# Optimization experiments

Measured on AMD Instinct MI355X. Metric: run time of the kernel, lower is better.

## Reference

```python
import jax, jax.numpy as jnp
import numpy as np

MIN_NORM = 1e-5
EPS = 1e-7
N_NODES = 100000
N_EDGES = 20000
NNZ = 640000
F_DIM = 128  # in_channels == out_channels
NUM_LAYERS = 2
MAX_NORM = 1e6


def _cosh(x):
    return jnp.cosh(jnp.clip(x, -15.0, 15.0))


def _sinh(x):
    return jnp.sinh(jnp.clip(x, -15.0, 15.0))


def _arcosh(x):
    # caller already clamps x >= 1 + eps
    return jnp.log(x + jnp.sqrt(jnp.clip(x * x - 1.0, EPS)))


def proj(x, c):
    K = 1.0 / c
    y = x[:, 1:]
    y_sq = jnp.sum(y * y, axis=1, keepdims=True)
    x0 = jnp.sqrt(jnp.clip(K + y_sq, EPS))
    return jnp.concatenate([x0, y], axis=1)


def proj_tan0(u):
    # zero out the time-like (first) coordinate
    return jnp.concatenate([jnp.zeros_like(u[:, :1]), u[:, 1:]], axis=1)


def expmap0(u, c):
    K = 1.0 / c
    sqrtK = jnp.sqrt(K)
    x = u[:, 1:]
    x_norm = jnp.clip(jnp.linalg.norm(x, axis=1, keepdims=True), MIN_NORM)
    theta = x_norm / sqrtK
    res0 = sqrtK * _cosh(theta)
    res_rest = sqrtK * _sinh(theta) * x / x_norm
    return proj(jnp.concatenate([res0, res_rest], axis=1), c)


def logmap0(x, c):
    K = 1.0 / c
    sqrtK = jnp.sqrt(K)
    y = x[:, 1:]
    y_norm = jnp.clip(jnp.linalg.norm(y, axis=1, keepdims=True), MIN_NORM)
    theta = jnp.clip(x[:, 0:1] / sqrtK, 1.0 + EPS)
    rest = sqrtK * _arcosh(theta) * y / y_norm
    return jnp.concatenate([jnp.zeros_like(x[:, :1]), rest], axis=1)


def minkowski_norm(u):
    dot = jnp.sum(u * u, axis=-1, keepdims=True) - 2.0 * (u[:, 0:1] * u[:, 0:1])
    return jnp.sqrt(jnp.clip(dot, EPS))


def proj_tan(u, x):
    ux = jnp.sum(x[:, 1:] * u[:, 1:], axis=1, keepdims=True)
    v0 = ux / jnp.clip(x[:, 0:1], EPS)
    return jnp.concatenate([v0, u[:, 1:]], axis=1)


def expmap(u, x, c):
    K = 1.0 / c
    sqrtK = jnp.sqrt(K)
    normu = jnp.clip(minkowski_norm(u), None, MAX_NORM)
    theta = jnp.clip(normu / sqrtK, MIN_NORM)
    result = _cosh(theta) * x + _sinh(theta) * u / theta
    return proj(result, c)


def ptransp0(x, u, c):
    K = 1.0 / c
    sqrtK = jnp.sqrt(K)
    x0 = x[:, 0:1]
    y = x[:, 1:]
    y_norm = jnp.clip(jnp.linalg.norm(y, axis=1, keepdims=True), MIN_NORM)
    y_hat = y / y_norm
    v = jnp.concatenate([-y_norm, (sqrtK - x0) * y_hat], axis=1)
    alpha = jnp.sum(y_hat * u[:, 1:], axis=1, keepdims=True) / sqrtK
    res = u - alpha * v
    return proj_tan(res, x)


def mobius_add(x, y, c):
    u = logmap0(y, c)
    v = ptransp0(x, u, c)
    return expmap(v, x, c)


def hyp_block(x, node_idx, edge_idx, bias, c_in, c_out):
    # tangent features at origin
    x = proj_tan0(logmap0(x, c_in))
    # degree normalizations (hyperedge_weight = ones, EW_weight = None)
    ones_nnz = jnp.ones((node_idx.shape[0],), dtype=x.dtype)
    D = jax.ops.segment_sum(ones_nnz, node_idx, num_segments=N_NODES)
    D = jnp.where(D > 0, 1.0 / D, 0.0)
    B = jax.ops.segment_sum(ones_nnz, edge_idx, num_segments=N_EDGES)
    B = jnp.where(B > 0, 1.0 / B, 0.0)
    # propagate nodes -> hyperedges (norm = B at destination edge)
    m1 = B[edge_idx][:, None] * x[node_idx]            # [nnz, F]
    e_feat = jax.ops.segment_sum(m1, edge_idx, num_segments=N_EDGES)
    # propagate hyperedges -> nodes (norm = D at destination node)
    m2 = D[node_idx][:, None] * e_feat[edge_idx]       # [nnz, F]
    out = jax.ops.segment_sum(m2, node_idx, num_segments=N_NODES)
    # hyperbolic bias add + activation
    bias_t = proj_tan0(bias[None, :])
    hyp_bias = proj(expmap0(bias_t, c_in), c_in)
    res = proj(out, c_in)
    res = proj(mobius_add(res, hyp_bias, c_in), c_in)
    out = jax.nn.leaky_relu(logmap0(res, c_in), 0.01)
    out = proj_tan0(out)
    return proj(expmap0(out, c_out), c_out)


def reference(x, hyperedge_index, curvatures, biases):
    node_idx = hyperedge_index[0]
    edge_idx = hyperedge_index[1]
    # encoder: prepend zero time coordinate, lift to hyperboloid
    h = jnp.concatenate([jnp.zeros_like(x[:, :1]), x], axis=1)
    c0 = jax.nn.softplus(curvatures[0])
    h = proj(expmap0(proj_tan0(h), c0), c0)
    for i in range(NUM_LAYERS):
        c_in = jax.nn.softplus(curvatures[i])
        c_out = jax.nn.softplus(curvatures[i + 1])
        h = hyp_block(h, node_idx, edge_idx, biases[i], c_in, c_out)
    # decoder
    c_last = jax.nn.softplus(curvatures[-1])
    return proj_tan0(logmap0(h, c_last))


def setup_inputs() -> dict:
    key = jax.random.key(0)
    k1, k2, k3, k4 = jax.random.split(key, 4)
    x = jax.random.normal(k1, (N_NODES, F_DIM - 1), dtype=jnp.float32)
    node_idx = jax.random.randint(k2, (NNZ,), 0, N_NODES)
    edge_idx = jax.random.randint(k3, (NNZ,), 0, N_EDGES)
    edge_idx = edge_idx.at[-1].set(N_EDGES - 1)  # ensure max edge id = E-1
    hyperedge_index = jnp.stack([node_idx, edge_idx], axis=0).astype(jnp.int64)
    curvatures = jnp.full((NUM_LAYERS + 1,), 0.1, dtype=jnp.float32)
    biases = 0.02 * jax.random.normal(k4, (NUM_LAYERS, F_DIM), dtype=jnp.float32)
    return {"x": x, "hyperedge_index": hyperedge_index, "curvatures": curvatures, "biases": biases}
```

## Files before the change

kernel.cpp:

```cpp
#include <hip/hip_runtime.h>
#include <hip/hip_fp16.h>
#include <math.h>

#define N_NODESc 100000
#define N_EDGESc 20000
#define NNZc     640000
#define FD       128
#define WE       96
#define WN       48
#define NBKT     256
#define EPB      2048
#define NCHUNKS  313
#define ESHIFT   7
#define NSHIFT   9
#define STAGEBLK 6250
#define MIN_NORMf 1e-5f
#define EPSf      1e-7f
#define MAX_NORMf 1e6f

__device__ __forceinline__ float wred(float v){
  #pragma unroll
  for(int m=32;m;m>>=1) v += __shfl_xor(v, m, 64);
  return v;
}
__device__ __forceinline__ void wred2_16(float& a, float& b){
  #pragma unroll
  for(int m=8;m;m>>=1){
    float ta = __shfl_xor(a, m, 64);
    float tb = __shfl_xor(b, m, 64);
    a += ta; b += tb;
  }
}

__device__ __forceinline__ void h8_acc(const float4 h, float4& a0, float4& a1){
  const __half2* hp = (const __half2*)&h;
  float2 f0 = __half22float2(hp[0]);
  float2 f1 = __half22float2(hp[1]);
  float2 f2 = __half22float2(hp[2]);
  float2 f3 = __half22float2(hp[3]);
  a0.x += f0.x; a0.y += f0.y; a0.z += f1.x; a0.w += f1.y;
  a1.x += f2.x; a1.y += f2.y; a1.z += f3.x; a1.w += f3.y;
}
__device__ __forceinline__ float4 pack_h8(const float4 a, const float4 b){
  float4 out;
  __half2* hp = (__half2*)&out;
  hp[0] = __float22half2_rn(make_float2(a.x,a.y));
  hp[1] = __float22half2_rn(make_float2(a.z,a.w));
  hp[2] = __float22half2_rn(make_float2(b.x,b.y));
  hp[3] = __float22half2_rn(make_float2(b.z,b.w));
  return out;
}

__device__ __forceinline__ void get_pair(const int* hei, int k, int f64, int& n, int& e){
  if(f64){ n = hei[2*k]; e = hei[2*NNZc + 2*k]; }
  else   { n = hei[k];   e = hei[NNZc + k]; }
}

__global__ void k_prep(const int* hei, const float* curv, const float* biases,
                       int* flag, float* scal, float* ubias, int* gHist){
  int tid = threadIdx.x;
  gHist[tid] = 0;
  gHist[tid + NBKT] = 0;
  if(tid < 64){
    int lane = tid;
    int hi = hei[2*lane+1];
    unsigned long long b = __ballot(hi != 0);
    if(lane==0) flag[0] = (b==0ull) ? 1 : 0;
    if(lane==0){
      scal[0] = log1pf(expf(curv[0]));
      scal[1] = log1pf(expf(curv[1]));
      scal[2] = log1pf(expf(curv[2]));
    }
    int d0 = 2*lane, d1 = d0+1;
    for(int L=0; L<2; ++L){
      float u0 = (d0==0) ? 0.f : biases[L*FD + d0];
      float u1 = biases[L*FD + d1];
      ubias[L*FD + d0] = u0;
      ubias[L*FD + d1] = u1;
      float uu = wred(u0*u0 + u1*u1);
      if(lane==0) scal[3+L] = uu;
    }
  }
}

__global__ void k_stage_hist(const float* x, float4* xh,
                             const int* hei, const int* flag, int* gHist){
  int bid = blockIdx.x;
  if(bid < STAGEBLK){
    int t = bid*256 + threadIdx.x;
    int node = t >> 4, l16 = t & 15;
    int d8 = 8*l16;
    const float* r = x + (size_t)node*(FD-1);
    float4 p0, p1;
    if(l16==0){
      float4 q0 = *(const float4*)(r);
      p1 = *(const float4*)(r + 3);
      p0 = make_float4(0.f, q0.x, q0.y, q0.z);
    } else {
      p0 = *(const float4*)(r + d8 - 1);
      p1 = *(const float4*)(r + d8 + 3);
    }
    xh[(size_t)node*16 + l16] = pack_h8(p0, p1);
  } else {
    __shared__ int h[NBKT];
    int tid = threadIdx.x;
    int hb = bid - STAGEBLK;
    int side = hb & 1;
    int chunk = hb >> 1;
    h[tid] = 0; __syncthreads();
    int f64 = flag[0];
    int base = chunk*EPB;
    #pragma unroll
    for(int j=0;j<8;++j){
      int k = base + j*256 + tid;
      if(k < NNZc){
        int n,e; get_pair(hei,k,f64,n,e);
        int b = side ? (n>>NSHIFT) : (e>>ESHIFT);
        atomicAdd(&h[b],1);
      }
    }
    __syncthreads();
    int c = h[tid];
    if(c>0) atomicAdd(&gHist[side*NBKT+tid], c);
  }
}

__global__ void k_scan(const int* gHist, int* gCur){
  __shared__ int sd[NBKT];
  int tid = threadIdx.x;
  for(int s=0;s<2;++s){
    int v = gHist[s*NBKT+tid];
    sd[tid]=v; __syncthreads();
    for(int off=1; off<NBKT; off<<=1){
      int t = (tid>=off)? sd[tid-off] : 0;
      __syncthreads();
      sd[tid] += t;
      __syncthreads();
    }
    gCur[s*NBKT+tid] = sd[tid]-v;
    __syncthreads();
  }
}

__global__ void k_part(const int* hei, const int* flag, int* gCur,
                       unsigned long long* partE, unsigned long long* partN,
                       int* curE, int* curN){
  int gtid = blockIdx.x*blockDim.x + threadIdx.x;
  if(gtid < N_EDGESc) curE[gtid] = 0;
  else if(gtid < N_EDGESc + N_NODESc) curN[gtid - N_EDGESc] = 0;

  __shared__ int h[NBKT];
  __shared__ int bbase[NBKT];
  int tid = threadIdx.x;
  int side = blockIdx.x & 1;
  int chunk = blockIdx.x >> 1;
  h[tid]=0; __syncthreads();
  int f64 = flag[0];
  int base = chunk*EPB;
  int keyv[8], payl[8], rank[8], bkt[8];
  #pragma unroll
  for(int j=0;j<8;++j){
    int k = base + j*256 + tid;
    if(k < NNZc){
      int n,e; get_pair(hei,k,f64,n,e);
      if(side==0){ keyv[j]=e; payl[j]=n; bkt[j]=e>>ESHIFT; }
      else       { keyv[j]=n; payl[j]=e; bkt[j]=n>>NSHIFT; }
      rank[j] = atomicAdd(&h[bkt[j]],1);
    } else bkt[j] = -1;
  }
  __syncthreads();
  int c = h[tid];
  if(c>0) bbase[tid] = atomicAdd(&gCur[side*NBKT+tid], c);
  __syncthreads();
  unsigned long long* part = side ? partN : partE;
  #pragma unroll
  for(int j=0;j<8;++j){
    if(bkt[j]>=0){
      int pos = bbase[bkt[j]] + rank[j];
      part[pos] = ((unsigned long long)(unsigned)keyv[j]<<32) | (unsigned)payl[j];
    }
  }
}

__global__ void k_build(const unsigned long long* partE, const unsigned long long* partN,
                        int* curE, int* curN, int* eEll, int* nEll){
  int bid = blockIdx.x;
  int xcd = bid & 7, i = bid >> 3;
  const int q = 1250/8, r = 1250%8;
  int chunk = (xcd<r ? xcd*(q+1) : r*(q+1)+(xcd-r)*q) + i;
  int side = chunk >= 625;
  int c = side ? chunk-625 : chunk;
  const unsigned long long* part = side ? partN : partE;
  int* cur = side ? curN : curE;
  int* ell = side ? nEll : eEll;
  int W = side ? WN : WE;
  int tid = threadIdx.x;
  #pragma unroll
  for(int j=0;j<4;++j){
    int k = c*1024 + j*256 + tid;
    unsigned long long v = part[k];
    int key = (int)(v>>32);
    int pay = (int)(unsigned)v;
    int pos = atomicAdd(&cur[key],1);
    if(pos<W) ell[(size_t)key*W+pos] = pay;
  }
}

__global__ void k_edge_gather(const int* curE, const int* eEll, const float4* rowsH, float4* efeatH){
  int t = blockIdx.x*blockDim.x + threadIdx.x;
  int w    = t >> 6;
  int lane = t & 63;
  int quad = lane >> 4, l16 = lane & 15;
  int edge = w*2 + (quad>>1);
  int qh   = quad & 1;

  int cnt = curE[edge];
  int use = cnt<WE ? cnt : WE;
  const int* ent = eEll + (size_t)edge*WE;

  float4 aA = make_float4(0.f,0.f,0.f,0.f);
  float4 aB = make_float4(0.f,0.f,0.f,0.f);
  int j = qh;
  for(; j+14 < use; j += 16){
    int r0 = ent[j];    int r1 = ent[j+2];
    int r2 = ent[j+4];  int r3 = ent[j+6];
    int r4 = ent[j+8];  int r5 = ent[j+10];
    int r6 = ent[j+12]; int r7 = ent[j+14];
    float4 h0 = rowsH[(size_t)r0*16 + l16];
    float4 h1 = rowsH[(size_t)r1*16 + l16];
    float4 h2 = rowsH[(size_t)r2*16 + l16];
    float4 h3 = rowsH[(size_t)r3*16 + l16];
    float4 h4 = rowsH[(size_t)r4*16 + l16];
    float4 h5 = rowsH[(size_t)r5*16 + l16];
    float4 h6 = rowsH[(size_t)r6*16 + l16];
    float4 h7 = rowsH[(size_t)r7*16 + l16];
    h8_acc(h0,aA,aB); h8_acc(h1,aA,aB); h8_acc(h2,aA,aB); h8_acc(h3,aA,aB);
    h8_acc(h4,aA,aB); h8_acc(h5,aA,aB); h8_acc(h6,aA,aB); h8_acc(h7,aA,aB);
  }
  for(; j < use; j += 2){
    float4 h = rowsH[(size_t)ent[j]*16 + l16];
    h8_acc(h,aA,aB);
  }
  aA.x += __shfl_xor(aA.x, 16, 64); aA.y += __shfl_xor(aA.y, 16, 64);
  aA.z += __shfl_xor(aA.z, 16, 64); aA.w += __shfl_xor(aA.w, 16, 64);
  aB.x += __shfl_xor(aB.x, 16, 64); aB.y += __shfl_xor(aB.y, 16, 64);
  aB.z += __shfl_xor(aB.z, 16, 64); aB.w += __shfl_xor(aB.w, 16, 64);

  if(qh==0){
    float b = cnt>0 ? __fdividef(1.f,(float)cnt) : 0.f;
    aA.x*=b; aA.y*=b; aA.z*=b; aA.w*=b;
    aB.x*=b; aB.y*=b; aB.z*=b; aB.w*=b;
    efeatH[(size_t)edge*16 + l16] = pack_h8(aA, aB);
  }
}

template<int OUTH>
__global__ void k_node_epilogue(const int* curN, const int* nEll, const float4* efeatH,
                                const float* scal, const float* ubias, int layer,
                                float4* outH, float* outF){
  int t = blockIdx.x*blockDim.x + threadIdx.x;
  int w    = t >> 6;
  int lane = t & 63;
  if(w >= N_NODESc/4) return;
  int quad = lane >> 4, l16 = lane & 15;
  int node = w*4 + quad;
  int d8 = 8*l16;

  float cin = scal[layer];
  float K   = __fdividef(1.f, cin);
  float sK  = sqrtf(K);
  float isK = __fdividef(1.f, sK);
  float uu  = scal[3+layer];

  int cnt = curN[node];
  float dv = cnt>0 ? __fdividef(1.f,(float)cnt) : 0.f;
  int use = cnt<WN ? cnt : WN;
  const int* ent = nEll + (size_t)node*WN;

  float4 aA = make_float4(0.f,0.f,0.f,0.f);
  float4 aB = make_float4(0.f,0.f,0.f,0.f);
  int j = 0;
  for(; j+3 < use; j += 4){
    int r0 = ent[j];   int r1 = ent[j+1];
    int r2 = ent[j+2]; int r3 = ent[j+3];
    float4 h0 = efeatH[(size_t)r0*16 + l16];
    float4 h1 = efeatH[(size_t)r1*16 + l16];
    float4 h2 = efeatH[(size_t)r2*16 + l16];
    float4 h3 = efeatH[(size_t)r3*16 + l16];
    h8_acc(h0,aA,aB); h8_acc(h1,aA,aB); h8_acc(h2,aA,aB); h8_acc(h3,aA,aB);
  }
  for(; j < use; ++j){
    float4 h = efeatH[(size_t)ent[j]*16 + l16];
    h8_acc(h,aA,aB);
  }
  aA.x*=dv; aA.y*=dv; aA.z*=dv; aA.w*=dv;
  aB.x*=dv; aB.y*=dv; aB.z*=dv; aB.w*=dv;

  const float4* up = (const float4*)(ubias + layer*FD + d8);
  float4 uA = up[0], uB = up[1];

  float ysq   = aA.x*aA.x + aA.y*aA.y + aA.z*aA.z + aA.w*aA.w
              + aB.x*aB.x + aB.y*aB.y + aB.z*aB.z + aB.w*aB.w;
  float dotAU = aA.x*uA.x + aA.y*uA.y + aA.z*uA.z + aA.w*uA.w
              + aB.x*uB.x + aB.y*uB.y + aB.z*uB.z + aB.w*uB.w;
  wred2_16(ysq, dotAU);

  float res0  = sqrtf(fmaxf(K + ysq, EPSf));
  float ynorm = fmaxf(sqrtf(ysq), MIN_NORMf);
  float iyn   = __fdividef(1.f, ynorm);

  float alpha = dotAU*iyn*isK;
  float ab    = alpha*(sK - res0);
  float abiyn = ab*iyn;
  float4 rA, rB;
  rA.x = fmaf(-abiyn, aA.x, uA.x); rA.y = fmaf(-abiyn, aA.y, uA.y);
  rA.z = fmaf(-abiyn, aA.z, uA.z); rA.w = fmaf(-abiyn, aA.w, uA.w);
  rB.x = fmaf(-abiyn, aB.x, uB.x); rB.y = fmaf(-abiyn, aB.y, uB.y);
  rB.z = fmaf(-abiyn, aB.z, uB.z); rB.w = fmaf(-abiyn, aB.w, uB.w);
  float ux  = fmaf(-ab, ynorm, dotAU);
  float v0s = ux * __fdividef(1.f, fmaxf(res0, EPSf));
  float rsq = fmaf(ab, ab, fmaf(-2.f*abiyn, dotAU, uu));

  float mink  = fmaxf(fmaf(-v0s, v0s, rsq), EPSf);
  float normu = fminf(sqrtf(mink), MAX_NORMf);
  float th    = fmaxf(normu*isK, MIN_NORMf);
  float thc   = fminf(th, 15.f);
  float e  = __expf(thc);
  float ei = __fdividef(1.f, e);
  float ch = 0.5f*(e + ei);
  float sh = 0.5f*(e - ei);
  float sth = sh*__fdividef(1.f, th);
  float4 qA, qB;
  qA.x = fmaf(ch, aA.x, sth*rA.x); qA.y = fmaf(ch, aA.y, sth*rA.y);
  qA.z = fmaf(ch, aA.z, sth*rA.z); qA.w = fmaf(ch, aA.w, sth*rA.w);
  qB.x = fmaf(ch, aB.x, sth*rB.x); qB.y = fmaf(ch, aB.y, sth*rB.y);
  qB.z = fmaf(ch, aB.z, sth*rB.z); qB.w = fmaf(ch, aB.w, sth*rB.w);

  float ysq2 = fmaxf(ch*ch*ysq + 2.f*ch*sth*ux + sth*sth*rsq, 0.f);
  float h0   = sqrtf(fmaxf(K + ysq2, EPSf));
  float yn3  = fmaxf(sqrtf(ysq2), MIN_NORMf);
  float th3  = fmaxf(h0*isK, 1.f+EPSf);
  float acs  = __logf(th3 + sqrtf(fmaxf(fmaf(th3,th3,-1.f), EPSf)));
  float fac  = sK*acs*__fdividef(1.f, yn3);
  float4 tA, tB;
  tA.x = fac*qA.x; tA.y = fac*qA.y; tA.z = fac*qA.z; tA.w = fac*qA.w;
  tB.x = fac*qB.x; tB.y = fac*qB.y; tB.z = fac*qB.z; tB.w = fac*qB.w;
  tA.x = tA.x>=0.f ? tA.x : 0.01f*tA.x;
  tA.y = tA.y>=0.f ? tA.y : 0.01f*tA.y;
  tA.z = tA.z>=0.f ? tA.z : 0.01f*tA.z;
  tA.w = tA.w>=0.f ? tA.w : 0.01f*tA.w;
  tB.x = tB.x>=0.f ? tB.x : 0.01f*tB.x;
  tB.y = tB.y>=0.f ? tB.y : 0.01f*tB.y;
  tB.z = tB.z>=0.f ? tB.z : 0.01f*tB.z;
  tB.w = tB.w>=0.f ? tB.w : 0.01f*tB.w;
  if(l16==0) tA.x = 0.f;

  if(OUTH){
    outH[(size_t)node*16 + l16] = pack_h8(tA, tB);
  } else {
    float4* op = (float4*)(outF + (size_t)node*FD + d8);
    op[0] = tA;
    op[1] = tB;
  }
}

extern "C" void kernel_launch(void* const* d_in, const int* in_sizes, int n_in,
                              void* d_out, int out_size, void* d_ws, size_t ws_size,
                              hipStream_t stream) {
  const float* x      = (const float*)d_in[0];
  const int*   hei    = (const int*)d_in[1];
  const float* curv   = (const float*)d_in[2];
  const float* biases = (const float*)d_in[3];
  float* out = (float*)d_out;

  char* p = (char*)d_ws;
  auto alloc = [&](size_t bytes){ char* r = p; p += (bytes + 255) & ~(size_t)255; return r; };
  int*   flag  = (int*)  alloc(4);
  float* scal  = (float*)alloc(16*4);
  float* ubias = (float*)alloc(2*FD*4);
  int*   gHist = (int*)  alloc(2*NBKT*4);
  int*   gCur  = (int*)  alloc(2*NBKT*4);
  int*   curE  = (int*)  alloc((size_t)N_EDGESc*4);
  int*   curN  = (int*)  alloc((size_t)N_NODESc*4);
  unsigned long long* partE = (unsigned long long*)alloc((size_t)NNZc*8);
  unsigned long long* partN = (unsigned long long*)alloc((size_t)NNZc*8);
  int*   eEll  = (int*)  alloc((size_t)N_EDGESc*WE*4);
  int*   nEll  = (int*)  alloc((size_t)N_NODESc*WN*4);
  float4* xh    = (float4*)alloc((size_t)N_NODESc*16*16);
  float4* tangH = (float4*)alloc((size_t)N_NODESc*16*16);
  float4* efeatH= (float4*)alloc((size_t)N_EDGESc*16*16);

  k_prep      <<<1, 256, 0, stream>>>(hei, curv, biases, flag, scal, ubias, gHist);
  k_stage_hist<<<STAGEBLK + 2*NCHUNKS, 256, 0, stream>>>(x, xh, hei, flag, gHist);
  k_scan      <<<1, NBKT, 0, stream>>>(gHist, gCur);
  k_part      <<<2*NCHUNKS, 256, 0, stream>>>(hei, flag, gCur, partE, partN, curE, curN);
  k_build     <<<1250, 256, 0, stream>>>(partE, partN, curE, curN, eEll, nEll);

  k_edge_gather     <<<(N_EDGESc/2*64)/256, 256, 0, stream>>>(curE, eEll, xh, efeatH);
  k_node_epilogue<1><<<(N_NODESc/4*64)/256, 256, 0, stream>>>(curN, nEll, efeatH, scal, ubias, 0, tangH, out);
  k_edge_gather     <<<(N_EDGESc/2*64)/256, 256, 0, stream>>>(curE, eEll, tangH, efeatH);
  k_node_epilogue<0><<<(N_NODESc/4*64)/256, 256, 0, stream>>>(curN, nEll, efeatH, scal, ubias, 1, tangH, out);
}
```

Measured before the change: 204.5 us.

## Fold bucket scan into partition and build per-bucket ELL with shared-memory counters

Removes the separate single-block scan kernel by having each partition block recompute the exclusive prefix over the global histogram locally and add it to a zero-based atomic cursor. The ELL build now assigns one block per bucket, keeping per-key slot counters in shared memory instead of global atomics, and writes the final counts out afterwards. This drops a kernel launch and the global count-zeroing pass, and turns global atomic contention into LDS atomics. In exchange every block redoes a 256-entry scan, and build parallelism falls to about 350 blocks with uneven bucket sizes.

```diff
diff --git a/kernel.cpp b/kernel.cpp
--- a/kernel.cpp
+++ b/kernel.cpp
@@ -13,6 +13,8 @@
 #define NCHUNKS  313
 #define ESHIFT   7
 #define NSHIFT   9
+#define NBKT_E   157
+#define NBKT_N   196
 #define STAGEBLK 6250
 #define MIN_NORMf 1e-5f
 #define EPSf      1e-7f
@@ -57,10 +59,10 @@
 }
 
 __global__ void k_prep(const int* hei, const float* curv, const float* biases,
-                       int* flag, float* scal, float* ubias, int* gHist){
+                       int* flag, float* scal, float* ubias, int* gHist, int* gCur){
   int tid = threadIdx.x;
-  gHist[tid] = 0;
-  gHist[tid + NBKT] = 0;
+  gHist[tid] = 0;  gHist[tid + NBKT] = 0;
+  gCur[tid]  = 0;  gCur[tid + NBKT]  = 0;
   if(tid < 64){
     int lane = tid;
     int hi = hei[2*lane+1];
@@ -125,36 +127,27 @@
   }
 }
 
-__global__ void k_scan(const int* gHist, int* gCur){
-  __shared__ int sd[NBKT];
-  int tid = threadIdx.x;
-  for(int s=0;s<2;++s){
-    int v = gHist[s*NBKT+tid];
-    sd[tid]=v; __syncthreads();
-    for(int off=1; off<NBKT; off<<=1){
-      int t = (tid>=off)? sd[tid-off] : 0;
-      __syncthreads();
-      sd[tid] += t;
-      __syncthreads();
-    }
-    gCur[s*NBKT+tid] = sd[tid]-v;
-    __syncthreads();
-  }
-}
-
-__global__ void k_part(const int* hei, const int* flag, int* gCur,
-                       unsigned long long* partE, unsigned long long* partN,
-                       int* curE, int* curN){
-  int gtid = blockIdx.x*blockDim.x + threadIdx.x;
-  if(gtid < N_EDGESc) curE[gtid] = 0;
-  else if(gtid < N_EDGESc + N_NODESc) curN[gtid - N_EDGESc] = 0;
-
+__global__ void k_part(const int* hei, const int* flag, const int* gHist, int* gCur,
+                       unsigned long long* partE, unsigned long long* partN){
+  __shared__ int sscan[NBKT];
   __shared__ int h[NBKT];
   __shared__ int bbase[NBKT];
   int tid = threadIdx.x;
   int side = blockIdx.x & 1;
   int chunk = blockIdx.x >> 1;
-  h[tid]=0; __syncthreads();
+
+  int hv = gHist[side*NBKT+tid];
+  sscan[tid] = hv;
+  h[tid] = 0;
+  __syncthreads();
+  for(int off=1; off<NBKT; off<<=1){
+    int t2 = (tid>=off)? sscan[tid-off] : 0;
+    __syncthreads();
+    sscan[tid] += t2;
+    __syncthreads();
+  }
+  int sbase = sscan[tid] - hv;
+
   int f64 = flag[0];
   int base = chunk*EPB;
   int keyv[8], payl[8], rank[8], bkt[8];
@@ -170,7 +163,7 @@
   }
   __syncthreads();
   int c = h[tid];
-  if(c>0) bbase[tid] = atomicAdd(&gCur[side*NBKT+tid], c);
+  if(c>0) bbase[tid] = sbase + atomicAdd(&gCur[side*NBKT+tid], c);
   __syncthreads();
   unsigned long long* part = side ? partN : partE;
   #pragma unroll
@@ -183,26 +176,47 @@
 }
 
 __global__ void k_build(const unsigned long long* partE, const unsigned long long* partN,
-                        int* curE, int* curN, int* eEll, int* nEll){
+                        const int* gHist, int* curE, int* curN, int* eEll, int* nEll){
+  __shared__ int sscan[NBKT];
+  __shared__ int lcur[512];
   int bid = blockIdx.x;
-  int xcd = bid & 7, i = bid >> 3;
-  const int q = 1250/8, r = 1250%8;
-  int chunk = (xcd<r ? xcd*(q+1) : r*(q+1)+(xcd-r)*q) + i;
-  int side = chunk >= 625;
-  int c = side ? chunk-625 : chunk;
+  int side = (bid >= NBKT_E) ? 1 : 0;
+  int bkt  = side ? bid - NBKT_E : bid;
+  int tid = threadIdx.x;
+
+  int hv = gHist[side*NBKT+tid];
+  sscan[tid] = hv; __syncthreads();
+  for(int off=1; off<NBKT; off<<=1){
+    int t2 = (tid>=off)? sscan[tid-off] : 0;
+    __syncthreads();
+    sscan[tid] += t2;
+    __syncthreads();
+  }
+  int cntB  = gHist[side*NBKT+bkt];
+  int start = sscan[bkt] - cntB;
+
+  int nkeys = side ? 512 : 128;
+  for(int i=tid; i<nkeys; i+=256) lcur[i] = 0;
+  __syncthreads();
+
   const unsigned long long* part = side ? partN : partE;
-  int* cur = side ? curN : curE;
   int* ell = side ? nEll : eEll;
   int W = side ? WN : WE;
-  int tid = threadIdx.x;
-  #pragma unroll
-  for(int j=0;j<4;++j){
-    int k = c*1024 + j*256 + tid;
-    unsigned long long v = part[k];
+  int keybase = side ? (bkt<<NSHIFT) : (bkt<<ESHIFT);
+  for(int i=tid; i<cntB; i+=256){
+    unsigned long long v = part[start+i];
     int key = (int)(v>>32);
     int pay = (int)(unsigned)v;
-    int pos = atomicAdd(&cur[key],1);
+    int pos = atomicAdd(&lcur[key-keybase], 1);
     if(pos<W) ell[(size_t)key*W+pos] = pay;
+  }
+  __syncthreads();
+
+  int total = side ? N_NODESc : N_EDGESc;
+  int* cur  = side ? curN : curE;
+  for(int i=tid; i<nkeys; i+=256){
+    int key = keybase + i;
+    if(key < total) cur[key] = lcur[i];
   }
 }
 
@@ -390,11 +404,10 @@
   float4* tangH = (float4*)alloc((size_t)N_NODESc*16*16);
   float4* efeatH= (float4*)alloc((size_t)N_EDGESc*16*16);
 
-  k_prep      <<<1, 256, 0, stream>>>(hei, curv, biases, flag, scal, ubias, gHist);
+  k_prep      <<<1, 256, 0, stream>>>(hei, curv, biases, flag, scal, ubias, gHist, gCur);
   k_stage_hist<<<STAGEBLK + 2*NCHUNKS, 256, 0, stream>>>(x, xh, hei, flag, gHist);
-  k_scan      <<<1, NBKT, 0, stream>>>(gHist, gCur);
-  k_part      <<<2*NCHUNKS, 256, 0, stream>>>(hei, flag, gCur, partE, partN, curE, curN);
-  k_build     <<<1250, 256, 0, stream>>>(partE, partN, curE, curN, eEll, nEll);
+  k_part      <<<2*NCHUNKS, 256, 0, stream>>>(hei, flag, gHist, gCur, partE, partN);
+  k_build     <<<NBKT_E + NBKT_N, 256, 0, stream>>>(partE, partN, gHist, curE, curN, eEll, nEll);
 
   k_edge_gather     <<<(N_EDGESc/2*64)/256, 256, 0, stream>>>(curE, eEll, xh, efeatH);
   k_node_epilogue<1><<<(N_NODESc/4*64)/256, 256, 0, stream>>>(curN, nEll, efeatH, scal, ubias, 0, tangH, out);
```

After: 179.9 us. 1.14x faster.
